# Kernel optimization log

Hardware: AMD Instinct MI355X
Metric: run time of the kernel (lower is better)

The kernel has to match this reference:

```python
import jax, jax.numpy as jnp
import numpy as np

ROPE_THETA = 10000.0

def apply_rope(x, pos):
    # x: [..., h, s, d], pos: [s] int positions
    d = x.shape[-1]
    inv_freq = ROPE_THETA ** (-jnp.arange(0, d, 2, dtype=jnp.float32) / d)  # [d/2]
    ang = pos.astype(jnp.float32)[:, None] * inv_freq[None, :]              # [s, d/2]
    cos, sin = jnp.cos(ang), jnp.sin(ang)
    x1, x2 = x[..., 0::2], x[..., 1::2]
    r1 = x1 * cos - x2 * sin
    r2 = x1 * sin + x2 * cos
    return jnp.stack([r1, r2], axis=-1).reshape(x.shape)

def setup_inputs() -> dict:
    key = jax.random.key(0)
    ks = jax.random.split(key, 5)
    B, S, D = 2, 2048, 1024
    scale = 1.0 / np.sqrt(D)
    return {
        "x": jax.random.normal(ks[0], (B, S, D), dtype=jnp.float32),
        "token_position": jnp.arange(S, dtype=jnp.int32),
        "Wq": jax.random.normal(ks[1], (D, D), dtype=jnp.float32) * scale,
        "Wk": jax.random.normal(ks[2], (D, D), dtype=jnp.float32) * scale,
        "Wv": jax.random.normal(ks[3], (D, D), dtype=jnp.float32) * scale,
        "Wo": jax.random.normal(ks[4], (D, D), dtype=jnp.float32) * scale,
    }

def reference(x, token_position, Wq, Wk, Wv, Wo):
    H = 16
    B, S, D = x.shape
    ds = D // H
    def split_heads(t):  # [b,s,(h d)] -> [b,h,s,d]
        return t.reshape(B, S, H, ds).transpose(0, 2, 1, 3)
    Q = split_heads(x @ Wq.T)
    K = split_heads(x @ Wk.T)
    V = split_heads(x @ Wv.T)
    Q = apply_rope(Q, token_position)
    K = apply_rope(K, token_position)
    scores = jnp.einsum('bhqd,bhkd->bhqk', Q, K) / jnp.sqrt(jnp.float32(ds))
    causal = jnp.tril(jnp.ones((S, S), dtype=bool))
    scores = jnp.where(causal, scores, jnp.finfo(scores.dtype).min)
    attn = jax.nn.softmax(scores, axis=-1)
    out = jnp.einsum('bhqk,bhkd->bhqd', attn, V)
    out = out.transpose(0, 2, 1, 3).reshape(B, S, D)
    return out @ Wo.T
```

## Files before the change

### kernel.cpp

```cpp
#include <hip/hip_runtime.h>
#include <math.h>

#define BB 2
#define SS 2048
#define DD 1024
#define HH 16
#define M_TOTAL (BB*SS)

typedef __attribute__((ext_vector_type(8))) short bf16x8;
typedef __attribute__((ext_vector_type(4))) float f32x4;

__device__ __forceinline__ short f2bf(float f) {
    union { float f; unsigned u; } v; v.f = f;
    unsigned r = v.u + 0x7fffu + ((v.u >> 16) & 1u);
    return (short)(r >> 16);
}
__device__ __forceinline__ float bf2f(short h) {
    union { unsigned u; float f; } v; v.u = ((unsigned)(unsigned short)h) << 16;
    return v.f;
}
__device__ __forceinline__ unsigned cvt_pk_bf16(float lo, float hi) {
    unsigned r;
    asm volatile("v_cvt_pk_bf16_f32 %0, %1, %2" : "=v"(r) : "v"(lo), "v"(hi));
    return r;
}
__device__ __forceinline__ void gload16(const void* g, void* l) {
    __builtin_amdgcn_global_load_lds(
        (const __attribute__((address_space(1))) unsigned int*)g,
        (__attribute__((address_space(3))) unsigned int*)l, 16, 0, 0);
}

__global__ __launch_bounds__(256) void cvt_all(const float* __restrict__ x,
                                               const float* __restrict__ wq,
                                               const float* __restrict__ wk,
                                               const float* __restrict__ wv,
                                               const float* __restrict__ wo,
                                               short* __restrict__ xb,
                                               short* __restrict__ wqb,
                                               short* __restrict__ wkb,
                                               short* __restrict__ wvb,
                                               short* __restrict__ wob,
                                               float qscale)
{
    const size_t T = (size_t)M_TOTAL * DD;
    const size_t W = (size_t)DD * DD;
    size_t i = ((size_t)blockIdx.x * 256 + threadIdx.x) * 4;
    const float* src; short* dst; float sc = 1.0f; size_t off;
    if (i < T)              { src = x;  dst = xb;  off = i; }
    else if (i < T + W)     { src = wq; dst = wqb; off = i - T; sc = qscale; }
    else if (i < T + 2*W)   { src = wk; dst = wkb; off = i - T - W; }
    else if (i < T + 3*W)   { src = wv; dst = wvb; off = i - T - 2*W; }
    else                    { src = wo; dst = wob; off = i - T - 3*W; }
    float4 v = *(const float4*)(src + off);
    short4 o;
    o.x = f2bf(v.x * sc); o.y = f2bf(v.y * sc);
    o.z = f2bf(v.z * sc); o.w = f2bf(v.w * sc);
    *(short4*)(dst + off) = o;
}

template<int BN, int OUT_BF16>
__global__ __launch_bounds__(256) void gemm_nt_mfma(const short* __restrict__ A,
                                                    const short* __restrict__ W0,
                                                    const short* __restrict__ W1,
                                                    const short* __restrict__ W2,
                                                    void* __restrict__ C0,
                                                    void* __restrict__ C1,
                                                    void* __restrict__ C2,
                                                    int M, int N, int K)
{
    constexpr int WC = BN / 64;
    constexpr int WR = 4 / WC;
    constexpr int MW = 128 / WR;
    constexpr int MT = MW / 16;

    __shared__ __align__(16) short As[128 * 64];
    __shared__ __align__(16) short Bs[BN * 64];

    const short* W = (blockIdx.z == 0) ? W0 : (blockIdx.z == 1) ? W1 : W2;
    void* Cout     = (blockIdx.z == 0) ? C0 : (blockIdx.z == 1) ? C1 : C2;

    const int tid = threadIdx.x;
    const int lane = tid & 63;
    const int w = tid >> 6;
    const int lg = lane >> 4, lc = lane & 15;
    const int wr = w / WC, wc = w % WC;
    const int m0 = blockIdx.y * 128, n0 = blockIdx.x * BN;
    const int wbase = (tid & 0xC0) * 8;

    f32x4 acc[MT][4] = {};

    for (int k0 = 0; k0 < K; k0 += 64) {
        __syncthreads();
#pragma unroll
        for (int it = 0; it < 4; ++it) {
            int cl = it * 256 + tid;
            int r = cl >> 3;
            int c = (cl & 7) ^ (r & 7);
            gload16(A + (size_t)(m0 + r) * K + k0 + c * 8, &As[it * 2048 + wbase]);
        }
#pragma unroll
        for (int it = 0; it < BN / 32; ++it) {
            int cl = it * 256 + tid;
            int r = cl >> 3;
            int c = (cl & 7) ^ (r & 7);
            gload16(W + (size_t)(n0 + r) * K + k0 + c * 8, &Bs[it * 2048 + wbase]);
        }
        __syncthreads();
#pragma unroll
        for (int ks = 0; ks < 2; ++ks) {
            bf16x8 af[MT], bfr[4];
#pragma unroll
            for (int mt = 0; mt < MT; ++mt) {
                int row = wr * MW + mt * 16 + lc;
                af[mt] = *(const bf16x8*)&As[row * 64 + (((ks * 4 + lg) ^ (row & 7)) * 8)];
            }
#pragma unroll
            for (int nt = 0; nt < 4; ++nt) {
                int row = wc * 64 + nt * 16 + lc;
                bfr[nt] = *(const bf16x8*)&Bs[row * 64 + (((ks * 4 + lg) ^ (row & 7)) * 8)];
            }
#pragma unroll
            for (int mt = 0; mt < MT; ++mt)
#pragma unroll
                for (int nt = 0; nt < 4; ++nt)
                    acc[mt][nt] = __builtin_amdgcn_mfma_f32_16x16x32_bf16(
                        af[mt], bfr[nt], acc[mt][nt], 0, 0, 0);
        }
    }
#pragma unroll
    for (int mt = 0; mt < MT; ++mt)
#pragma unroll
        for (int nt = 0; nt < 4; ++nt)
#pragma unroll
            for (int rg = 0; rg < 4; ++rg) {
                int row = m0 + wr * MW + mt * 16 + lg * 4 + rg;
                int col = n0 + wc * 64 + nt * 16 + lc;
                if (OUT_BF16)
                    ((short*)Cout)[(size_t)row * N + col] = f2bf(acc[mt][nt][rg]);
                else
                    ((float*)Cout)[(size_t)row * N + col] = acc[mt][nt][rg];
            }
}

__global__ __launch_bounds__(256) void rope_qk(short* __restrict__ Q,
                                               short* __restrict__ K,
                                               const int* __restrict__ pos)
{
    const int t = blockIdx.x * 256 + threadIdx.x;
    const int ig = t & 7;
    const int h = (t >> 3) & 15;
    const int s = (t >> 7) & 2047;
    const int b = t >> 18;
    const float p = (float)pos[s];
    const size_t off = ((size_t)(b * SS + s)) * DD + h * 64 + ig * 8;
    bf16x8 q8 = *(bf16x8*)(Q + off);
    bf16x8 k8 = *(bf16x8*)(K + off);
#pragma unroll
    for (int j = 0; j < 4; ++j) {
        int i = ig * 4 + j;
        float ang = p * __expf(-(float)i * (9.210340371976184f / 32.0f));
        float c = cosf(ang), sn = sinf(ang);
        float q1 = bf2f(q8[2 * j]), q2 = bf2f(q8[2 * j + 1]);
        q8[2 * j]     = f2bf(q1 * c - q2 * sn);
        q8[2 * j + 1] = f2bf(q1 * sn + q2 * c);
        float k1 = bf2f(k8[2 * j]), k2 = bf2f(k8[2 * j + 1]);
        k8[2 * j]     = f2bf(k1 * c - k2 * sn);
        k8[2 * j + 1] = f2bf(k1 * sn + k2 * c);
    }
    *(bf16x8*)(Q + off) = q8;
    *(bf16x8*)(K + off) = k8;
}

__global__ __launch_bounds__(256) void attn_mfma(const short* __restrict__ Q,
                                                 const short* __restrict__ K,
                                                 const short* __restrict__ V,
                                                 short* __restrict__ O)
{
    __shared__ __align__(16) short Ks[2][64 * 64];
    __shared__ __align__(16) unsigned Vt32[2][64 * 36];
    __shared__ __align__(16) unsigned Pl32[4][16 * 36];

    const int tid = threadIdx.x;
    const int lane = tid & 63;
    const int w = tid >> 6;
    const int lg = lane >> 4, lc = lane & 15;

    const int bid = blockIdx.x;
    const int qt = 31 - (bid >> 5);
    const int bh = bid & 31;
    const int b = bh >> 4, h = bh & 15;

    const short* Qh = Q + (size_t)b * SS * DD + h * 64;
    const short* Kh = K + (size_t)b * SS * DD + h * 64;
    const short* Vh = V + (size_t)b * SS * DD + h * 64;
    short* Oh = O + (size_t)b * SS * DD + h * 64;

    const int qg = qt * 64 + w * 16 + lc;
    bf16x8 qa[2];
#pragma unroll
    for (int ks = 0; ks < 2; ++ks)
        qa[ks] = *(const bf16x8*)(Qh + (size_t)qg * DD + ks * 32 + lg * 8);

    f32x4 oaccT[4] = {};
    float l = 0.0f;

    const int vc = tid & 7, vrp = tid >> 3;
    unsigned* Pw = &Pl32[w][0];
    const int kbase_lds = (tid & 0xC0) * 8;

    {
        bf16x8 v0 = *(const bf16x8*)(Vh + (size_t)(2 * vrp) * DD + vc * 8);
        bf16x8 v1 = *(const bf16x8*)(Vh + (size_t)(2 * vrp + 1) * DD + vc * 8);
#pragma unroll
        for (int it = 0; it < 2; ++it) {
            int cl = it * 256 + tid;
            int r = cl >> 3;
            int c = (cl & 7) ^ (r & 7);
            gload16(Kh + (size_t)r * DD + c * 8, &Ks[0][it * 2048 + kbase_lds]);
        }
#pragma unroll
        for (int j = 0; j < 8; ++j) {
            int ds = vc * 8 + j;
            unsigned pk = (unsigned)(unsigned short)v0[j] |
                          ((unsigned)(unsigned short)v1[j] << 16);
            Vt32[0][ds * 36 + (vrp ^ (vc << 2))] = pk;
        }
    }
    __syncthreads();
    int cur = 0;

    for (int kt = 0; kt <= qt; ++kt) {
        bf16x8 v0n, v1n;
        const bool more = (kt < qt);
        if (more) {
            const int nv0 = (kt + 1) * 64;
            v0n = *(const bf16x8*)(Vh + (size_t)(nv0 + 2 * vrp) * DD + vc * 8);
            v1n = *(const bf16x8*)(Vh + (size_t)(nv0 + 2 * vrp + 1) * DD + vc * 8);
#pragma unroll
            for (int it = 0; it < 2; ++it) {
                int cl = it * 256 + tid;
                int r = cl >> 3;
                int c = (cl & 7) ^ (r & 7);
                gload16(Kh + (size_t)(nv0 + r) * DD + c * 8,
                        &Ks[cur ^ 1][it * 2048 + kbase_lds]);
            }
        }

        f32x4 s[4] = {};
        __builtin_amdgcn_s_setprio(1);
#pragma unroll
        for (int ks = 0; ks < 2; ++ks) {
            int c2 = ks * 4 + lg;
#pragma unroll
            for (int t = 0; t < 4; ++t) {
                int kr = t * 16 + lc;
                bf16x8 kb = *(const bf16x8*)&Ks[cur][kr * 64 + ((c2 ^ (kr & 7)) * 8)];
                s[t] = __builtin_amdgcn_mfma_f32_16x16x32_bf16(kb, qa[ks], s[t], 0, 0, 0);
            }
        }
        __builtin_amdgcn_s_setprio(0);

        if (kt == qt) {
            const int kv0 = kt * 64;
#pragma unroll
            for (int t = 0; t < 4; ++t)
#pragma unroll
                for (int rg = 0; rg < 4; ++rg)
                    if (kv0 + t * 16 + lg * 4 + rg > qg) s[t][rg] = -1e30f;
        }

#pragma unroll
        for (int t = 0; t < 4; ++t) {
            float p0 = exp2f(s[t][0]);
            float p1 = exp2f(s[t][1]);
            float p2 = exp2f(s[t][2]);
            float p3 = exp2f(s[t][3]);
            l += (p0 + p1) + (p2 + p3);
            uint2 pk;
            pk.x = cvt_pk_bf16(p0, p1);
            pk.y = cvt_pk_bf16(p2, p3);
            *(uint2*)&Pw[lc * 36 + 8 * t + 2 * lg] = pk;
        }

        __builtin_amdgcn_s_setprio(1);
#pragma unroll
        for (int ks = 0; ks < 2; ++ks) {
            bf16x8 pb = *(const bf16x8*)&Pw[lc * 36 + 16 * ks + 4 * lg];
#pragma unroll
            for (int dt = 0; dt < 4; ++dt) {
                int vr = dt * 16 + lc;
                bf16x8 vb = *(const bf16x8*)&Vt32[cur][vr * 36 +
                                4 * ((ks * 4 + lg) ^ ((vr >> 3) & 7))];
                oaccT[dt] = __builtin_amdgcn_mfma_f32_16x16x32_bf16(vb, pb, oaccT[dt], 0, 0, 0);
            }
        }
        __builtin_amdgcn_s_setprio(0);

        if (more) {
#pragma unroll
            for (int j = 0; j < 8; ++j) {
                int ds = vc * 8 + j;
                unsigned pk = (unsigned)(unsigned short)v0n[j] |
                              ((unsigned)(unsigned short)v1n[j] << 16);
                Vt32[cur ^ 1][ds * 36 + (vrp ^ (vc << 2))] = pk;
            }
        }
        __syncthreads();
        cur ^= 1;
    }

    l += __shfl_xor(l, 16);
    l += __shfl_xor(l, 32);
    const float inv = 1.0f / l;
#pragma unroll
    for (int dt = 0; dt < 4; ++dt)
#pragma unroll
        for (int rg = 0; rg < 4; ++rg)
            Oh[(size_t)qg * DD + dt * 16 + lg * 4 + rg] = f2bf(oaccT[dt][rg] * inv);
}

extern "C" void kernel_launch(void* const* d_in, const int* in_sizes, int n_in,
                              void* d_out, int out_size, void* d_ws, size_t ws_size,
                              hipStream_t stream)
{
    const float* x   = (const float*)d_in[0];
    const int*   pos = (const int*)d_in[1];
    const float* Wq  = (const float*)d_in[2];
    const float* Wk  = (const float*)d_in[3];
    const float* Wv  = (const float*)d_in[4];
    const float* Wo  = (const float*)d_in[5];
    float* out = (float*)d_out;

    const size_t T = (size_t)M_TOTAL * DD;
    const size_t WSZ = (size_t)DD * DD;
    short* xb  = (short*)d_ws;
    short* wqb = xb + T;
    short* wkb = wqb + WSZ;
    short* wvb = wkb + WSZ;
    short* wob = wvb + WSZ;
    short* Qb  = wob + WSZ;
    short* Kb  = Qb + T;
    short* Vb  = Kb + T;
    short* AOb = Vb + T;

    const int cvt_blocks = (int)((T + 4 * WSZ) / 1024);
    cvt_all<<<cvt_blocks, 256, 0, stream>>>(x, Wq, Wk, Wv, Wo,
                                            xb, wqb, wkb, wvb, wob,
                                            0.18033688011112042f);

    dim3 gqkv(DD / 128, M_TOTAL / 128, 3);
    gemm_nt_mfma<128, 1><<<gqkv, 256, 0, stream>>>(
        xb, wqb, wkb, wvb, Qb, Kb, Vb, M_TOTAL, DD, DD);

    rope_qk<<<(BB * SS * HH * 8) / 256, 256, 0, stream>>>(Qb, Kb, pos);

    attn_mfma<<<BB * HH * (SS / 64), 256, 0, stream>>>(Qb, Kb, Vb, AOb);

    dim3 go(DD / 64, M_TOTAL / 128, 1);
    gemm_nt_mfma<64, 0><<<go, 256, 0, stream>>>(
        AOb, wob, wob, wob, (void*)out, (void*)out, (void*)out, M_TOTAL, DD, DD);
}
```

Baseline: 113.8 us.

## Process two 64-row query tiles per attention block to reuse K/V tiles

Each attention block now handles 128 query rows (two 64-row groups per wave set) instead of 64, so every K and V tile staged in shared memory feeds twice as many MFMAs. This halves the global K/V loads and LDS staging per query row, and halves the grid. In exchange it doubles the accumulator and score registers, which may lower occupancy. It also wastes work on the upper-diagonal tile for the first query group and leaves fewer blocks to balance the causal load.

Result: slower. 126.9 us (+11.6%).

```diff
diff --git a/kernel.cpp b/kernel.cpp
--- a/kernel.cpp
+++ b/kernel.cpp
@@ -178,7 +178,7 @@
 {
     __shared__ __align__(16) short Ks[2][64 * 64];
     __shared__ __align__(16) unsigned Vt32[2][64 * 36];
-    __shared__ __align__(16) unsigned Pl32[4][16 * 36];
+    __shared__ __align__(16) unsigned Pl32[4][2][16 * 36];
 
     const int tid = threadIdx.x;
     const int lane = tid & 63;
@@ -186,7 +186,7 @@
     const int lg = lane >> 4, lc = lane & 15;
 
     const int bid = blockIdx.x;
-    const int qt = 31 - (bid >> 5);
+    const int qt = 15 - (bid >> 5);
     const int bh = bid & 31;
     const int b = bh >> 4, h = bh & 15;
 
@@ -195,18 +195,23 @@
     const short* Vh = V + (size_t)b * SS * DD + h * 64;
     short* Oh = O + (size_t)b * SS * DD + h * 64;
 
-    const int qg = qt * 64 + w * 16 + lc;
-    bf16x8 qa[2];
-#pragma unroll
-    for (int ks = 0; ks < 2; ++ks)
-        qa[ks] = *(const bf16x8*)(Qh + (size_t)qg * DD + ks * 32 + lg * 8);
-
-    f32x4 oaccT[4] = {};
-    float l = 0.0f;
+    const int qg0 = qt * 128 + w * 16 + lc;
+    const int qg1 = qg0 + 64;
+    bf16x8 qa[2][2];
+#pragma unroll
+    for (int ks = 0; ks < 2; ++ks) {
+        qa[0][ks] = *(const bf16x8*)(Qh + (size_t)qg0 * DD + ks * 32 + lg * 8);
+        qa[1][ks] = *(const bf16x8*)(Qh + (size_t)qg1 * DD + ks * 32 + lg * 8);
+    }
+
+    f32x4 oaccT[2][4] = {};
+    float l0 = 0.0f, l1 = 0.0f;
 
     const int vc = tid & 7, vrp = tid >> 3;
-    unsigned* Pw = &Pl32[w][0];
+    unsigned* Pw0 = &Pl32[w][0][0];
+    unsigned* Pw1 = &Pl32[w][1][0];
     const int kbase_lds = (tid & 0xC0) * 8;
+    const int nkt = 2 * qt + 2;
 
     {
         bf16x8 v0 = *(const bf16x8*)(Vh + (size_t)(2 * vrp) * DD + vc * 8);
@@ -229,9 +234,9 @@
     __syncthreads();
     int cur = 0;
 
-    for (int kt = 0; kt <= qt; ++kt) {
+    for (int kt = 0; kt < nkt; ++kt) {
         bf16x8 v0n, v1n;
-        const bool more = (kt < qt);
+        const bool more = (kt + 1 < nkt);
         if (more) {
             const int nv0 = (kt + 1) * 64;
             v0n = *(const bf16x8*)(Vh + (size_t)(nv0 + 2 * vrp) * DD + vc * 8);
@@ -246,7 +251,7 @@
             }
         }
 
-        f32x4 s[4] = {};
+        f32x4 s[2][4] = {};
         __builtin_amdgcn_s_setprio(1);
 #pragma unroll
         for (int ks = 0; ks < 2; ++ks) {
@@ -255,43 +260,58 @@
             for (int t = 0; t < 4; ++t) {
                 int kr = t * 16 + lc;
                 bf16x8 kb = *(const bf16x8*)&Ks[cur][kr * 64 + ((c2 ^ (kr & 7)) * 8)];
-                s[t] = __builtin_amdgcn_mfma_f32_16x16x32_bf16(kb, qa[ks], s[t], 0, 0, 0);
+                s[0][t] = __builtin_amdgcn_mfma_f32_16x16x32_bf16(kb, qa[0][ks], s[0][t], 0, 0, 0);
+                s[1][t] = __builtin_amdgcn_mfma_f32_16x16x32_bf16(kb, qa[1][ks], s[1][t], 0, 0, 0);
             }
         }
         __builtin_amdgcn_s_setprio(0);
 
-        if (kt == qt) {
+        if (kt >= 2 * qt) {
             const int kv0 = kt * 64;
 #pragma unroll
             for (int t = 0; t < 4; ++t)
 #pragma unroll
-                for (int rg = 0; rg < 4; ++rg)
-                    if (kv0 + t * 16 + lg * 4 + rg > qg) s[t][rg] = -1e30f;
+                for (int rg = 0; rg < 4; ++rg) {
+                    int key = kv0 + t * 16 + lg * 4 + rg;
+                    if (key > qg0) s[0][t][rg] = -1e30f;
+                    if (key > qg1) s[1][t][rg] = -1e30f;
+                }
         }
 
 #pragma unroll
         for (int t = 0; t < 4; ++t) {
-            float p0 = exp2f(s[t][0]);
-            float p1 = exp2f(s[t][1]);
-            float p2 = exp2f(s[t][2]);
-            float p3 = exp2f(s[t][3]);
-            l += (p0 + p1) + (p2 + p3);
-            uint2 pk;
-            pk.x = cvt_pk_bf16(p0, p1);
-            pk.y = cvt_pk_bf16(p2, p3);
-            *(uint2*)&Pw[lc * 36 + 8 * t + 2 * lg] = pk;
+            float a0 = exp2f(s[0][t][0]);
+            float a1 = exp2f(s[0][t][1]);
+            float a2 = exp2f(s[0][t][2]);
+            float a3 = exp2f(s[0][t][3]);
+            l0 += (a0 + a1) + (a2 + a3);
+            uint2 pk0;
+            pk0.x = cvt_pk_bf16(a0, a1);
+            pk0.y = cvt_pk_bf16(a2, a3);
+            *(uint2*)&Pw0[lc * 36 + 8 * t + 2 * lg] = pk0;
+            float b0 = exp2f(s[1][t][0]);
+            float b1 = exp2f(s[1][t][1]);
+            float b2 = exp2f(s[1][t][2]);
+            float b3 = exp2f(s[1][t][3]);
+            l1 += (b0 + b1) + (b2 + b3);
+            uint2 pk1;
+            pk1.x = cvt_pk_bf16(b0, b1);
+            pk1.y = cvt_pk_bf16(b2, b3);
+            *(uint2*)&Pw1[lc * 36 + 8 * t + 2 * lg] = pk1;
         }
 
         __builtin_amdgcn_s_setprio(1);
 #pragma unroll
         for (int ks = 0; ks < 2; ++ks) {
-            bf16x8 pb = *(const bf16x8*)&Pw[lc * 36 + 16 * ks + 4 * lg];
+            bf16x8 pb0 = *(const bf16x8*)&Pw0[lc * 36 + 16 * ks + 4 * lg];
+            bf16x8 pb1 = *(const bf16x8*)&Pw1[lc * 36 + 16 * ks + 4 * lg];
 #pragma unroll
             for (int dt = 0; dt < 4; ++dt) {
                 int vr = dt * 16 + lc;
                 bf16x8 vb = *(const bf16x8*)&Vt32[cur][vr * 36 +
                                 4 * ((ks * 4 + lg) ^ ((vr >> 3) & 7))];
-                oaccT[dt] = __builtin_amdgcn_mfma_f32_16x16x32_bf16(vb, pb, oaccT[dt], 0, 0, 0);
+                oaccT[0][dt] = __builtin_amdgcn_mfma_f32_16x16x32_bf16(vb, pb0, oaccT[0][dt], 0, 0, 0);
+                oaccT[1][dt] = __builtin_amdgcn_mfma_f32_16x16x32_bf16(vb, pb1, oaccT[1][dt], 0, 0, 0);
             }
         }
         __builtin_amdgcn_s_setprio(0);
@@ -309,14 +329,19 @@
         cur ^= 1;
     }
 
-    l += __shfl_xor(l, 16);
-    l += __shfl_xor(l, 32);
-    const float inv = 1.0f / l;
+    l0 += __shfl_xor(l0, 16);
+    l0 += __shfl_xor(l0, 32);
+    l1 += __shfl_xor(l1, 16);
+    l1 += __shfl_xor(l1, 32);
+    const float inv0 = 1.0f / l0;
+    const float inv1 = 1.0f / l1;
 #pragma unroll
     for (int dt = 0; dt < 4; ++dt)
 #pragma unroll
-        for (int rg = 0; rg < 4; ++rg)
-            Oh[(size_t)qg * DD + dt * 16 + lg * 4 + rg] = f2bf(oaccT[dt][rg] * inv);
+        for (int rg = 0; rg < 4; ++rg) {
+            Oh[(size_t)qg0 * DD + dt * 16 + lg * 4 + rg] = f2bf(oaccT[0][dt][rg] * inv0);
+            Oh[(size_t)qg1 * DD + dt * 16 + lg * 4 + rg] = f2bf(oaccT[1][dt][rg] * inv1);
+        }
 }
 
 extern "C" void kernel_launch(void* const* d_in, const int* in_sizes, int n_in,
@@ -354,7 +379,7 @@
 
     rope_qk<<<(BB * SS * HH * 8) / 256, 256, 0, stream>>>(Qb, Kb, pos);
 
-    attn_mfma<<<BB * HH * (SS / 64), 256, 0, stream>>>(Qb, Kb, Vb, AOb);
+    attn_mfma<<<BB * HH * (SS / 128), 256, 0, stream>>>(Qb, Kb, Vb, AOb);
 
     dim3 go(DD / 64, M_TOTAL / 128, 1);
     gemm_nt_mfma<64, 0><<<go, 256, 0, stream>>>(
```
